# Kernel tuning notes

Hardware: AMD Instinct MI355X
Metric: run time of the kernel (lower is better)

## Reference

```python
import jax, jax.numpy as jnp
from jax import lax
import numpy as np

DN = ('NCHW', 'OIHW', 'NCHW')

def _conv(x, w, b, s):
    # torch Conv2d(kernel=3, padding=1, stride=s)
    y = lax.conv_general_dilated(x, w, (s, s), ((1, 1), (1, 1)), dimension_numbers=DN)
    return y + b[None, :, None, None]

def _convT(x, w, b, s):
    # torch ConvTranspose2d weight layout [in, out, kh, kw]; kernel=3, padding=1, output_padding=s-1
    wk = jnp.flip(w, (2, 3)).transpose(1, 0, 2, 3)  # -> OIHW
    y = lax.conv_general_dilated(x, wk, (1, 1), ((1, s), (1, s)), lhs_dilation=(s, s), dimension_numbers=DN)
    return y + b[None, :, None, None]

def _inorm(x, eps=1e-5):
    # torch InstanceNorm2d (affine=False)
    m = jnp.mean(x, (2, 3), keepdims=True)
    v = jnp.var(x, (2, 3), keepdims=True)
    return (x - m) * lax.rsqrt(v + eps)

def _prelu(x, a):
    return jnp.where(x >= 0, x, a * x)

def _block(x, w, b, a, s):
    return _prelu(_inorm(_conv(x, w, b, s)), a)

def _sage(x, src, tgt, wl, bl, wr, n):
    # PyG SAGEConv, mean aggregation: lin_l(scatter_mean(x[src] -> tgt)) + lin_r(x)
    deg = jnp.zeros((n,), x.dtype).at[tgt].add(1.0)
    agg = jnp.zeros((x.shape[0], n, x.shape[2]), x.dtype).at[:, tgt].add(x[:, src])
    agg = agg / jnp.maximum(deg, 1.0)[None, :, None]
    return jnp.einsum('bnc,oc->bno', agg, wl) + bl + jnp.einsum('bnc,oc->bno', x, wr)

def setup_inputs() -> dict:
    keys = iter(jax.random.split(jax.random.key(0), 64))
    def rn(shape, s=0.05):
        return jax.random.normal(next(keys), shape, jnp.float32) * s
    inp = {}
    inp['x'] = jax.random.normal(next(keys), (16, 1, 400, 400), jnp.float32)
    inp['edges'] = jax.random.randint(next(keys), (2, 5000), 0, 625, jnp.int32)
    for name, (ci, co) in zip(['d4', 'd3', 'd2', 'd1'], [(1, 32), (32, 64), (64, 128), (128, 256)]):
        inp['w_' + name] = rn((co, ci, 3, 3)); inp['b_' + name] = rn((co,))
        inp['a_' + name] = jnp.full((1,), 0.25, jnp.float32)
    inp['w_bot'] = rn((256, 256, 3, 3)); inp['b_bot'] = rn((256,))
    inp['a_bot'] = jnp.full((1,), 0.25, jnp.float32)
    for i in ['1', '2']:
        inp['wl' + i] = rn((256, 256)); inp['bl' + i] = rn((256,)); inp['wr' + i] = rn((256, 256))
    for name, (ci, co) in zip(['u1', 'u2', 'u3'], [(512, 128), (256, 64), (128, 32)]):
        inp['w_' + name] = rn((ci, co, 3, 3)); inp['b_' + name] = rn((co,))
        inp['a_' + name] = jnp.full((1,), 0.25, jnp.float32)
    inp['w_u4'] = rn((64, 2, 3, 3)); inp['b_u4'] = rn((2,))
    return inp

def reference(x, edges, w_d4, b_d4, a_d4, w_d3, b_d3, a_d3, w_d2, b_d2, a_d2, w_d1, b_d1, a_d1, w_bot, b_bot, a_bot, wl1, bl1, wr1, wl2, bl2, wr2, w_u1, b_u1, a_u1, w_u2, b_u2, a_u2, w_u3, b_u3, a_u3, w_u4, b_u4):
    xs = []
    x = _block(x, w_d4, b_d4, a_d4, 2); xs.append(x)   # [B,32,200,200]
    x = _block(x, w_d3, b_d3, a_d3, 2); xs.append(x)   # [B,64,100,100]
    x = _block(x, w_d2, b_d2, a_d2, 2); xs.append(x)   # [B,128,50,50]
    x = _block(x, w_d1, b_d1, a_d1, 2); xs.append(x)   # [B,256,25,25]
    x = _block(x, w_bot, b_bot, a_bot, 1)              # [B,256,25,25]
    B = x.shape[0]
    x = x.reshape(B, 256, -1).transpose(0, 2, 1)       # [B,625,256]
    src, tgt = edges[0], edges[1]
    x = jax.nn.relu(_sage(x, src, tgt, wl1, bl1, wr1, 625))
    x = jax.nn.relu(_sage(x, src, tgt, wl2, bl2, wr2, 625))
    x = x.transpose(0, 2, 1).reshape(B, 256, 25, 25)
    x = jnp.concatenate([xs[3], x], 1)                 # 512 ch
    x = _prelu(_inorm(_convT(x, w_u1, b_u1, 2)), a_u1) # [B,128,50,50]
    x = jnp.concatenate([xs[2], x], 1)
    x = _prelu(_inorm(_convT(x, w_u2, b_u2, 2)), a_u2) # [B,64,100,100]
    x = jnp.concatenate([xs[1], x], 1)
    x = _prelu(_inorm(_convT(x, w_u3, b_u3, 2)), a_u3) # [B,32,200,200]
    x = jnp.concatenate([xs[0], x], 1)
    return _convT(x, w_u4, b_u4, 2)                    # [B,2,400,400], conv_only top
```

## Files before the change

kernel.cpp:

```cpp
#include <hip/hip_runtime.h>
#include <hip/hip_bf16.h>

typedef __hip_bfloat16 bf16;

typedef __bf16 bf16x8 __attribute__((ext_vector_type(8)));
typedef float  f32x16 __attribute__((ext_vector_type(16)));

static __device__ __forceinline__ float bf(const bf16 v){ return __bfloat162float(v); }
static __device__ __forceinline__ float bfu(unsigned short u){
  unsigned fw = ((unsigned)u) << 16; float v; __builtin_memcpy(&v, &fw, 4); return v;
}

static __device__ __forceinline__ float ldm(const void* p, long i, int f){
  return f ? ((const float*)p)[i] : __bfloat162float(((const bf16*)p)[i]);
}
static __device__ __forceinline__ void stm(void* p, long i, int f, float v){
  if(f) ((float*)p)[i] = v; else ((bf16*)p)[i] = __float2bfloat16(v);
}
static __device__ __forceinline__ unsigned short bfbits(float v){
  __hip_bfloat16 h = __float2bfloat16(v);
  return *(unsigned short*)&h;
}

__global__ void k_detect(const void* __restrict__ w, int* __restrict__ mode){
  if(blockIdx.x == 0 && threadIdx.x == 0){
    const unsigned int* u = (const unsigned int*)w;
    int saneLo = 0;
    for(int i = 0; i < 64; i++){
      unsigned short lo = (unsigned short)(u[i] & 0xFFFFu);
      unsigned int fw = ((unsigned int)lo) << 16;
      float v; __builtin_memcpy(&v, &fw, 4);
      float a = fabsf(v);
      if(a > 1e-7f && a < 100.f) saneLo++;
    }
    *mode = (saneLo >= 48) ? 0 : 1;
  }
}

__global__ void k_wtrans6(const void* __restrict__ w, bf16* __restrict__ wF,
                          const int* __restrict__ dmode){
  int idx = blockIdx.x * 256 + threadIdx.x;
  if(idx >= 65536) return;
  int dm = *dmode;
  int e = idx & 7;
  int L = (idx >> 3) & 63;
  int r = idx >> 9;
  int nc = r & 7;
  int kc = r >> 3;
  int o = nc*32 + (L & 31);
  int c = kc*16 + (L >> 5)*8 + e;
  wF[idx] = __float2bfloat16(ldm(w, (long)o*256 + c, dm));
}

__global__ void k_wtrans4(const void* __restrict__ w, bf16* __restrict__ wF,
                          const int* __restrict__ dmode, int Cin, int Cout){
  int idx = blockIdx.x * 256 + threadIdx.x;
  if(idx >= Cin * Cout * 9) return;
  int dm = *dmode;
  int e = idx & 7;
  int L = (idx >> 3) & 63;
  int r = idx >> 9;
  int NC = Cout >> 5;
  int nc = r % NC; r /= NC;
  int t  = r % 9;
  int kc = r / 9;
  int ci = kc*16 + (L>>5)*8 + e;
  int co = nc*32 + (L&31);
  wF[idx] = __float2bfloat16(ldm(w, ((long)ci*Cout + co)*9 + t, dm));
}

__global__ void k_wtrans5(const void* __restrict__ w, bf16* __restrict__ wF,
                          const int* __restrict__ dmode, int Cin, int Cout){
  int idx = blockIdx.x * 256 + threadIdx.x;
  if(idx >= Cin * Cout * 9) return;
  int dm = *dmode;
  int e = idx & 7;
  int L = (idx >> 3) & 63;
  int r = idx >> 9;
  int NC = Cout >> 5;
  int nc = r % NC; r /= NC;
  int t  = r % 9;
  int kc = r / 9;
  int ci = kc*16 + (L>>5)*8 + e;
  int co = nc*32 + (L&31);
  wF[idx] = __float2bfloat16(ldm(w, ((long)co*Cin + ci)*9 + t, dm));
}

__global__ void k_count(const int* __restrict__ tgt, int* __restrict__ icur, int E){
  int e = blockIdx.x * 256 + threadIdx.x;
  if(e < E) atomicAdd(&icur[tgt[e]], 1);
}
__global__ void k_scan(int* __restrict__ icur, int* __restrict__ off, int N){
  if(blockIdx.x == 0 && threadIdx.x == 0){
    int acc = 0;
    for(int i = 0; i < N; i++){ off[i] = acc; acc += icur[i]; icur[i] = 0; }
    off[N] = acc;
  }
}
__global__ void k_place(const int* __restrict__ src, const int* __restrict__ tgt,
                        const int* __restrict__ off, int* __restrict__ icur,
                        int* __restrict__ eidx, int E){
  int e = blockIdx.x * 256 + threadIdx.x;
  if(e < E){
    int d = tgt[e];
    int p = atomicAdd(&icur[d], 1);
    eidx[off[d] + p] = src[e];
  }
}

__global__ __launch_bounds__(256, 4)
void k_conv_d4(const void* __restrict__ in, long in_off,
               const void* __restrict__ w, const void* __restrict__ bias,
               bf16* __restrict__ out, const int* __restrict__ dmode)
{
  __shared__ float sW[288];
  __shared__ float sB[32];
  int tid = threadIdx.x;
  int dm = *dmode;
  for(int e = tid; e < 288; e += 256) sW[e] = ldm(w, e, dm);
  if(tid < 32)  sB[tid] = ldm(bias, tid, dm);
  __syncthreads();
  int r = tid / 50, jt = tid % 50;
  if(r >= 5) return;
  int ho = blockIdx.x * 5 + r;
  int b  = blockIdx.z;
  int j0 = jt * 4;

  float x[3][9];
  long ibase = in_off + (long)b * 160000;
  #pragma unroll
  for(int rr = 0; rr < 3; rr++){
    int ir = 2*ho - 1 + rr;
    if(ir < 0 || ir >= 400){
      #pragma unroll
      for(int c = 0; c < 9; c++) x[rr][c] = 0.f;
      continue;
    }
    long rb = ibase + (long)ir * 400;
    int c0 = 2*j0 - 1;
    #pragma unroll
    for(int c = 0; c < 9; c++){
      int ic = c0 + c;
      x[rr][c] = (ic >= 0 && ic < 400) ? ldm(in, rb + ic, dm) : 0.f;
    }
  }

  long obase = ((long)b * 32) * 40000 + (long)ho * 200 + j0;
  for(int co = 0; co < 32; co++){
    const float* wv = &sW[co*9];
    float bv = sB[co];
    float a[4];
    #pragma unroll
    for(int p = 0; p < 4; p++){
      float s = bv;
      #pragma unroll
      for(int kh = 0; kh < 3; kh++)
        #pragma unroll
        for(int kw = 0; kw < 3; kw++)
          s += x[kh][2*p + kw] * wv[kh*3 + kw];
      a[p] = s;
    }
    ushort4 pk;
    pk.x = bfbits(a[0]); pk.y = bfbits(a[1]); pk.z = bfbits(a[2]); pk.w = bfbits(a[3]);
    *(ushort4*)&out[obase + (long)co * 40000] = pk;
  }
}

template<int CW, int NWC, int NWM, int S, int OCC, int VECW>
__global__ __launch_bounds__(256, OCC)
void k_convSM(const void* __restrict__ in, long in_off, int fin_sel,
              const bf16* __restrict__ wF, const void* __restrict__ bias,
              void* __restrict__ out, int fout,
              const int* __restrict__ dmode,
              int Cin, int Hin, int Win, int Cout, int Hout, int Wout, int nym)
{
  constexpr int CP = 40;
  constexpr int HALF = CW/2;
  __shared__ unsigned short sX[3*CW*CP];
  int tid  = threadIdx.x;
  int lane = tid & 63;
  int wv   = tid >> 6;
  int nc   = wv % NWC;
  int mt   = wv / NWC;
  int ho   = blockIdx.x;
  int colg = blockIdx.y % nym;
  int cog  = blockIdx.y / nym;
  int b    = blockIdx.z;
  int dm   = *dmode;
  int fin  = (fin_sel == 2) ? dm : fin_sel;
  int NCtot = Cout >> 5;
  int chunk = cog*NWC + nc;
  int jl   = mt*32 + (lane & 31);
  int hi   = lane >> 5;
  int C0   = S*(colg*NWM*32);
  int ir0  = S*ho - 1;

  f32x16 acc;
  #pragma unroll
  for(int q = 0; q < 16; q++) acc[q] = 0.f;

  int p0, p1, p2;
  if(S == 2){ p0 = jl; p1 = HALF + jl; p2 = jl + 1; }
  else      { p0 = jl; p1 = jl + 1;    p2 = jl + 2; }

  for(int ci0 = 0; ci0 < Cin; ci0 += 32){
    if(VECW == 1){
      for(int e = tid; e < 12*CW; e += 256){
        int c  = e % CW;
        int s  = e / CW;
        int kg = s & 3, r = s >> 2;
        int ir = ir0 + r;
        int ic = C0 - 1 + c;
        unsigned pk0, pk1, pk2, pk3;
        if(ir >= 0 && ir < Hin && ic >= 0 && ic < Win){
          long step = (long)Hin*Win;
          long base = in_off + ((long)b*Cin + ci0 + kg*8)*step + (long)ir*Win + ic;
          unsigned short t8[8];
          #pragma unroll
          for(int u = 0; u < 8; u++) t8[u] = bfbits(ldm(in, base + u*step, fin));
          pk0 = t8[0] | ((unsigned)t8[1]<<16);
          pk1 = t8[2] | ((unsigned)t8[3]<<16);
          pk2 = t8[4] | ((unsigned)t8[5]<<16);
          pk3 = t8[6] | ((unsigned)t8[7]<<16);
        } else { pk0=0; pk1=0; pk2=0; pk3=0; }
        int pos = (S == 2) ? ((c&1) ? HALF + (c>>1) : (c>>1)) : c;
        uint4 q; q.x=pk0; q.y=pk1; q.z=pk2; q.w=pk3;
        *(uint4*)&sX[(r*CW + pos)*CP + kg*8] = q;
      }
    } else {
      const unsigned short* bp = (const unsigned short*)in;
      long step = (long)Hin*Win;
      int L0 = (C0 >= 1) ? ((C0-1) & ~(VECW-1)) : -VECW;
      int ng = (C0 + CW - 2 - L0)/VECW + 1;
      int total = 3 * 8 * ng;
      for(int e = tid; e < total; e += 256){
        int c4 = e & 7;
        int s  = e >> 3;
        int g  = s % ng;
        int r  = s / ng;
        int ir = ir0 + r;
        int L  = L0 + g*VECW;
        int cib = ci0 + c4*4;
        unsigned short t[4][VECW];
        if(ir >= 0 && ir < Hin && L >= 0 && L + VECW <= Win){
          const unsigned short* rp = bp + in_off + ((long)b*Cin + cib)*step + (long)ir*Win + L;
          #pragma unroll
          for(int u = 0; u < 4; u++){
            if(VECW == 4){
              ushort4 v = *(const ushort4*)(rp + u*step);
              t[u][0]=v.x; t[u][1]=v.y; t[u][2]=v.z; t[u][3]=v.w;
            } else {
              ushort2 v = *(const ushort2*)(rp + u*step);
              t[u][0]=v.x; t[u][1]=v.y;
            }
          }
        } else {
          #pragma unroll
          for(int j = 0; j < VECW; j++){
            int ic = L + j;
            bool ok = (ir >= 0 && ir < Hin && ic >= 0 && ic < Win);
            #pragma unroll
            for(int u = 0; u < 4; u++)
              t[u][j] = ok ? bp[in_off + ((long)b*Cin + cib+u)*step + (long)ir*Win + ic]
                           : (unsigned short)0;
          }
        }
        #pragma unroll
        for(int j = 0; j < VECW; j++){
          int c = L - C0 + 1 + j;
          if(c < 0 || c >= CW) continue;
          int pos = (S == 2) ? ((c&1) ? HALF + (c>>1) : (c>>1)) : c;
          uint2 q;
          q.x = t[0][j] | ((unsigned)t[1][j]<<16);
          q.y = t[2][j] | ((unsigned)t[3][j]<<16);
          *(uint2*)&sX[(r*CW + pos)*CP + c4*4] = q;
        }
      }
    }
    __syncthreads();

    #pragma unroll
    for(int kg2 = 0; kg2 < 2; kg2++){
      int kbase = 8*hi + kg2*16;
      bf16x8 x[9];
      #pragma unroll
      for(int r = 0; r < 3; r++){
        x[r*3+0] = *(const bf16x8*)&sX[(r*CW + p0)*CP + kbase];
        x[r*3+1] = *(const bf16x8*)&sX[(r*CW + p1)*CP + kbase];
        x[r*3+2] = *(const bf16x8*)&sX[(r*CW + p2)*CP + kbase];
      }
      int kc = (ci0 >> 4) + kg2;
      const bf16x8* wb = ((const bf16x8*)wF) + ((long)(kc*9)*NCtot + chunk)*64 + lane;
      const long ws = (long)NCtot*64;
      #pragma unroll
      for(int t = 0; t < 9; t++){
        bf16x8 w = wb[(long)t*ws];
        acc = __builtin_amdgcn_mfma_f32_32x32x16_bf16(w, x[t], acc, 0,0,0);
      }
    }
    __syncthreads();
  }

  int j = colg*NWM*32 + jl;
  if(j < Wout){
    #pragma unroll
    for(int r16 = 0; r16 < 16; r16++){
      int co = chunk*32 + (r16&3) + 8*(r16>>2) + 4*hi;
      float bv = ldm(bias, co, dm);
      stm(out, ((long)b*Cout + co)*Hout*Wout + (long)ho*Wout + j, fout, acc[r16] + bv);
    }
  }
}

__global__ void k_inorm_prelu(void* __restrict__ x, int f, int HW,
                              const void* __restrict__ a, const int* __restrict__ dmode)
{
  int dm = *dmode;
  long base = (long)blockIdx.x * HW;
  float s = 0.f, s2 = 0.f;
  int vec = (f == 0) && ((HW & 3) == 0);
  if(vec){
    const ushort4* vp = (const ushort4*)((const bf16*)x + base);
    int n = HW >> 2;
    for(int i = threadIdx.x; i < n; i += 256){
      ushort4 v = vp[i];
      float a0 = bfu(v.x), a1 = bfu(v.y), a2 = bfu(v.z), a3 = bfu(v.w);
      s  += (a0 + a1) + (a2 + a3);
      s2 += (a0*a0 + a1*a1) + (a2*a2 + a3*a3);
    }
  } else {
    for(int i = threadIdx.x; i < HW; i += 256){ float v = ldm(x, base + i, f); s += v; s2 += v*v; }
  }
  __shared__ float sh[256], sh2[256];
  sh[threadIdx.x] = s; sh2[threadIdx.x] = s2; __syncthreads();
  for(int off = 128; off > 0; off >>= 1){
    if(threadIdx.x < off){ sh[threadIdx.x] += sh[threadIdx.x+off]; sh2[threadIdx.x] += sh2[threadIdx.x+off]; }
    __syncthreads();
  }
  float mean = sh[0] / HW;
  float var  = sh2[0] / HW - mean * mean;
  float inv  = rsqrtf(fmaxf(var, 0.f) + 1e-5f);
  float alpha = ldm(a, 0, dm);
  if(vec){
    ushort4* vp = (ushort4*)((bf16*)x + base);
    int n = HW >> 2;
    for(int i = threadIdx.x; i < n; i += 256){
      ushort4 v = vp[i];
      float t[4] = { bfu(v.x), bfu(v.y), bfu(v.z), bfu(v.w) };
      #pragma unroll
      for(int k = 0; k < 4; k++){
        float u = (t[k] - mean) * inv;
        t[k] = u >= 0.f ? u : alpha * u;
      }
      ushort4 o;
      o.x = bfbits(t[0]); o.y = bfbits(t[1]); o.z = bfbits(t[2]); o.w = bfbits(t[3]);
      vp[i] = o;
    }
  } else {
    for(int i = threadIdx.x; i < HW; i += 256){
      float v = (ldm(x, base + i, f) - mean) * inv;
      stm(x, base + i, f, v >= 0.f ? v : alpha * v);
    }
  }
}

__global__ void k_transpose(const float* __restrict__ in, float* __restrict__ out, int B, int C, int N){
  long idx = (long)blockIdx.x * 256 + threadIdx.x;
  long total = (long)B * C * N; if(idx >= total) return;
  int c = (int)(idx % C); long t = idx / C; int n = (int)(t % N); int b = (int)(t / N);
  out[idx] = in[((long)b * C + c) * N + n];
}

__global__ __launch_bounds__(256, 4)
void k_sageG(const float* __restrict__ xT,
             const int* __restrict__ off, const int* __restrict__ eidx,
             const bf16* __restrict__ wlF, const bf16* __restrict__ wrF,
             const void* __restrict__ bl,
             float* __restrict__ out, const int* __restrict__ dmode,
             int NROW, int trans)
{
  constexpr int CP = 264;
  __shared__ unsigned short sS[2*32*CP];
  int tid  = threadIdx.x;
  int lane = tid & 63;
  int wv   = tid >> 6;
  int ln   = lane & 31;
  int hi   = lane >> 5;
  int n0   = blockIdx.x * 32;
  int og0  = blockIdx.y * 128;
  int ncg  = blockIdx.y*4 + wv;
  int dm   = *dmode;

  for(int e = tid; e < 4096; e += 256){
    int c4 = e & 63;
    int r  = (e >> 6) & 31;
    int ar = e >> 11;
    int row = n0 + r;
    unsigned pk0 = 0, pk1 = 0;
    if(row < NROW){
      float4 v;
      if(ar == 0){
        v = *(const float4*)&xT[(long)row*256 + c4*4];
      } else {
        int b = row / 625;
        int n = row - b*625;
        int s0 = off[n], s1 = off[n+1];
        v.x = 0.f; v.y = 0.f; v.z = 0.f; v.w = 0.f;
        long bb = (long)b*625*256 + c4*4;
        for(int k = s0; k < s1; k++){
          int s = eidx[k];
          float4 u = *(const float4*)&xT[bb + (long)s*256];
          v.x += u.x; v.y += u.y; v.z += u.z; v.w += u.w;
        }
        float dinv = 1.0f / fmaxf((float)(s1 - s0), 1.0f);
        v.x *= dinv; v.y *= dinv; v.z *= dinv; v.w *= dinv;
      }
      pk0 = bfbits(v.x) | ((unsigned)bfbits(v.y) << 16);
      pk1 = bfbits(v.z) | ((unsigned)bfbits(v.w) << 16);
    }
    uint2 q; q.x = pk0; q.y = pk1;
    *(uint2*)&sS[(ar*32 + r)*CP + c4*4] = q;
  }
  __syncthreads();

  f32x16 acc;
  #pragma unroll
  for(int q = 0; q < 16; q++) acc[q] = 0.f;

  int xb = ln*CP + 8*hi;
  #pragma unroll
  for(int kc = 0; kc < 16; kc++){
    bf16x8 bx = *(const bf16x8*)&sS[xb + kc*16];
    bf16x8 ba = *(const bf16x8*)&sS[32*CP + xb + kc*16];
    bf16x8 wl = ((const bf16x8*)wlF)[(long)(kc*8 + ncg)*64 + lane];
    bf16x8 wr = ((const bf16x8*)wrF)[(long)(kc*8 + ncg)*64 + lane];
    acc = __builtin_amdgcn_mfma_f32_32x32x16_bf16(wl, ba, acc, 0,0,0);
    acc = __builtin_amdgcn_mfma_f32_32x32x16_bf16(wr, bx, acc, 0,0,0);
  }

  if(trans){
    int row = n0 + ln;
    if(row < NROW){
      int b = row / 625, n = row - b*625;
      #pragma unroll
      for(int r16 = 0; r16 < 16; r16++){
        int o = ncg*32 + (r16&3) + 8*(r16>>2) + 4*hi;
        float v = acc[r16] + ldm(bl, o, dm);
        out[((long)b*256 + o)*625 + n] = fmaxf(v, 0.f);
      }
    }
  } else {
    float* sO = (float*)sS;
    __syncthreads();
    #pragma unroll
    for(int r16 = 0; r16 < 16; r16++){
      int ol = wv*32 + (r16&3) + 8*(r16>>2) + 4*hi;
      float v = acc[r16] + ldm(bl, og0 + ol, dm);
      sO[ln*130 + ol] = fmaxf(v, 0.f);
    }
    __syncthreads();
    for(int e = tid; e < 4096; e += 256){
      int r = e >> 7, oc = e & 127;
      int row = n0 + r;
      if(row < NROW) out[(long)row*256 + og0 + oc] = sO[r*130 + oc];
    }
  }
}

template<int CW, int NWC, int NWM, int CC, int CIP, int VECW>
__global__ __launch_bounds__(512, 4)
void k_convTG(const void* __restrict__ inA, int fA,
              const void* __restrict__ inB, int fB,
              const bf16* __restrict__ wF, const void* __restrict__ bias,
              bf16* __restrict__ out, const int* __restrict__ dmode,
              int Hin, int Win, int Cout)
{
  __shared__ unsigned short sX[4*CW*CIP];
  int tid  = threadIdx.x;
  int lane = tid & 63;
  int wv   = tid >> 6;
  int low  = wv & 3;
  int h    = wv >> 2;
  int nc   = low % NWC;
  int mt   = low / NWC;
  int j0   = mt * 32;
  int i    = blockIdx.x;
  int b    = blockIdx.z;
  int dm   = *dmode;
  int ln   = lane & 31;
  int hi   = lane >> 5;
  int NCtot = Cout >> 5;

  f32x16 acc0, acc1, acc2, acc3;
  #pragma unroll
  for(int q = 0; q < 16; q++){ acc0[q]=0.f; acc1[q]=0.f; acc2[q]=0.f; acc3[q]=0.f; }

  if(VECW == 1){
    for(int e = tid; e < 4*CW*(CC/8); e += 512){
      int col = e % CW;
      int s   = e / CW;
      int kg  = s % (CC/8); s /= (CC/8);
      int row = s & 1;
      int hf  = s >> 1;
      int ii  = i + row;
      unsigned pk0=0, pk1=0, pk2=0, pk3=0;
      if(ii < Hin && col < Win){
        const void* sp = hf ? inB : inA;
        int ff = hf ? fB : fA;
        long step = (long)Hin*Win;
        long base = ((long)b*CC + kg*8)*step + (long)ii*Win + col;
        unsigned short t8[8];
        #pragma unroll
        for(int u = 0; u < 8; u++) t8[u] = bfbits(ldm(sp, base + u*step, ff));
        pk0 = t8[0] | ((unsigned)t8[1]<<16);
        pk1 = t8[2] | ((unsigned)t8[3]<<16);
        pk2 = t8[4] | ((unsigned)t8[5]<<16);
        pk3 = t8[6] | ((unsigned)t8[7]<<16);
      }
      uint4 q; q.x=pk0; q.y=pk1; q.z=pk2; q.w=pk3;
      *(uint4*)&sX[((hf*2 + row)*CW + col)*CIP + kg*8] = q;
    }
  } else {
    long step = (long)Hin*Win;
    constexpr int NG = (CW + VECW - 1)/VECW;
    constexpr int NC4 = CC/4;
    int total = 4 * NC4 * NG;
    for(int e = tid; e < total; e += 512){
      int c4 = e % NC4;
      int s  = e / NC4;
      int g  = s % NG; s /= NG;
      int row = s & 1;
      int hf  = s >> 1;
      int ii  = i + row;
      int col0 = g*VECW;
      const unsigned short* bp = (const unsigned short*)(hf ? inB : inA);
      unsigned short t[4][VECW];
      if(ii < Hin && col0 + VECW <= Win){
        const unsigned short* rp = bp + ((long)b*CC + c4*4)*step + (long)ii*Win + col0;
        #pragma unroll
        for(int u = 0; u < 4; u++){
          if(VECW == 4){
            ushort4 v = *(const ushort4*)(rp + u*step);
            t[u][0]=v.x; t[u][1]=v.y; t[u][2]=v.z; t[u][3]=v.w;
          } else {
            ushort2 v = *(const ushort2*)(rp + u*step);
            t[u][0]=v.x; t[u][1]=v.y;
          }
        }
      } else {
        #pragma unroll
        for(int j = 0; j < VECW; j++){
          int ic = col0 + j;
          bool ok = (ii < Hin && ic < Win);
          #pragma unroll
          for(int u = 0; u < 4; u++)
            t[u][j] = ok ? bp[((long)b*CC + c4*4+u)*step + (long)ii*Win + ic]
                         : (unsigned short)0;
        }
      }
      #pragma unroll
      for(int j = 0; j < VECW; j++){
        int c = col0 + j;
        if(c >= CW) continue;
        uint2 q;
        q.x = t[0][j] | ((unsigned)t[1][j]<<16);
        q.y = t[2][j] | ((unsigned)t[3][j]<<16);
        *(uint2*)&sX[((hf*2 + row)*CW + c)*CIP + c4*4] = q;
      }
    }
  }
  __syncthreads();

  for(int kc = 0; kc < CC/16; kc++){
    int kb = kc*16 + 8*hi;
    bf16x8 x00 = *(const bf16x8*)&sX[((h*2+0)*CW + j0 + ln)*CIP + kb];
    bf16x8 x01 = *(const bf16x8*)&sX[((h*2+0)*CW + j0 + ln + 1)*CIP + kb];
    bf16x8 x10 = *(const bf16x8*)&sX[((h*2+1)*CW + j0 + ln)*CIP + kb];
    bf16x8 x11 = *(const bf16x8*)&sX[((h*2+1)*CW + j0 + ln + 1)*CIP + kb];
    int kcg = h*(CC/16) + kc;
    const bf16x8* wb = ((const bf16x8*)wF) + ((long)(kcg*9)*NCtot + nc)*64 + lane;
    const int ws = NCtot*64;
    bf16x8 w0=wb[0],    w1=wb[ws],   w2=wb[2*ws], w3=wb[3*ws], w4=wb[4*ws],
           w5=wb[5*ws], w6=wb[6*ws], w7=wb[7*ws], w8=wb[8*ws];
    acc0 = __builtin_amdgcn_mfma_f32_32x32x16_bf16(w4, x00, acc0, 0,0,0);
    acc1 = __builtin_amdgcn_mfma_f32_32x32x16_bf16(w5, x00, acc1, 0,0,0);
    acc1 = __builtin_amdgcn_mfma_f32_32x32x16_bf16(w3, x01, acc1, 0,0,0);
    acc2 = __builtin_amdgcn_mfma_f32_32x32x16_bf16(w7, x00, acc2, 0,0,0);
    acc2 = __builtin_amdgcn_mfma_f32_32x32x16_bf16(w1, x10, acc2, 0,0,0);
    acc3 = __builtin_amdgcn_mfma_f32_32x32x16_bf16(w8, x00, acc3, 0,0,0);
    acc3 = __builtin_amdgcn_mfma_f32_32x32x16_bf16(w6, x01, acc3, 0,0,0);
    acc3 = __builtin_amdgcn_mfma_f32_32x32x16_bf16(w2, x10, acc3, 0,0,0);
    acc3 = __builtin_amdgcn_mfma_f32_32x32x16_bf16(w0, x11, acc3, 0,0,0);
  }

  float* sR = (float*)sX;
  __syncthreads();
  if(h == 1){
    #pragma unroll
    for(int q = 0; q < 16; q++){
      sR[(0*16+q)*256 + low*64 + lane] = acc0[q];
      sR[(1*16+q)*256 + low*64 + lane] = acc1[q];
      sR[(2*16+q)*256 + low*64 + lane] = acc2[q];
      sR[(3*16+q)*256 + low*64 + lane] = acc3[q];
    }
  }
  __syncthreads();
  if(h == 0){
    #pragma unroll
    for(int q = 0; q < 16; q++){
      acc0[q] += sR[(0*16+q)*256 + low*64 + lane];
      acc1[q] += sR[(1*16+q)*256 + low*64 + lane];
      acc2[q] += sR[(2*16+q)*256 + low*64 + lane];
      acc3[q] += sR[(3*16+q)*256 + low*64 + lane];
    }
    int j = j0 + ln;
    if(j < Win){
      int Wout = 2*Win;
      #pragma unroll
      for(int r = 0; r < 16; r++){
        int co = nc*32 + (r&3) + 8*(r>>2) + 4*hi;
        float bv = ldm(bias, co, dm);
        long base0 = (((long)b*Cout + co)*2*Hin + 2*i)*(long)Wout + 2*j;
        unsigned p0 = bfbits(acc0[r]+bv) | ((unsigned)bfbits(acc1[r]+bv) << 16);
        unsigned p1 = bfbits(acc2[r]+bv) | ((unsigned)bfbits(acc3[r]+bv) << 16);
        *(unsigned*)&out[base0]        = p0;
        *(unsigned*)&out[base0 + Wout] = p1;
      }
    }
  }
}

__global__ __launch_bounds__(256, 4)
void k_convT8(const bf16* __restrict__ inA, const bf16* __restrict__ inB,
              const void* __restrict__ w, const void* __restrict__ bias,
              void* __restrict__ out, long out_off, int fout_sel,
              const int* __restrict__ dmode, int Hin, int Win)
{
  __shared__ float sW[64*2*9];
  __shared__ float sB[2];
  int tid = threadIdx.x;
  int dm = *dmode;
  for(int e = tid; e < 64*2*9; e += 256) sW[e] = ldm(w, e, dm);
  if(tid < 2) sB[tid] = ldm(bias, tid, dm);
  __syncthreads();
  int r  = tid / 50;
  int jt = tid % 50;
  if(r >= 5) return;
  int i  = blockIdx.x * 5 + r;
  int b  = blockIdx.z;
  int j0 = jt * 4;
  int fout = (fout_sel == 2) ? dm : fout_sel;

  float acc[2][4][4];
  #pragma unroll
  for(int co = 0; co < 2; co++)
    #pragma unroll
    for(int p = 0; p < 4; p++){
      acc[co][p][0]=0.f; acc[co][p][1]=0.f; acc[co][p][2]=0.f; acc[co][p][3]=0.f;
    }

  bool e4   = (j0 + 4 < Win);
  bool row1 = (i + 1 < Hin);

  for(int ci = 0; ci < 64; ci++){
    const bf16* src = (ci < 32) ? inA : inB;
    int cc = ci & 31;
    const bf16* rp = src + ((long)b*32 + cc)*(long)Hin*Win + (long)i*Win + j0;
    float x0[5], x1[5];
    ushort4 v0 = *(const ushort4*)rp;
    x0[0]=bfu(v0.x); x0[1]=bfu(v0.y); x0[2]=bfu(v0.z); x0[3]=bfu(v0.w);
    x0[4] = e4 ? bf(rp[4]) : 0.f;
    if(row1){
      ushort4 v1 = *(const ushort4*)(rp + Win);
      x1[0]=bfu(v1.x); x1[1]=bfu(v1.y); x1[2]=bfu(v1.z); x1[3]=bfu(v1.w);
      x1[4] = e4 ? bf(rp[Win + 4]) : 0.f;
    } else {
      x1[0]=0.f; x1[1]=0.f; x1[2]=0.f; x1[3]=0.f; x1[4]=0.f;
    }
    const float* wp = &sW[ci*18];
    float wv[18];
    #pragma unroll
    for(int k = 0; k < 18; k++) wv[k] = wp[k];
    #pragma unroll
    for(int p = 0; p < 4; p++){
      float a00 = x0[p], a01 = x0[p+1], a10 = x1[p], a11 = x1[p+1];
      #pragma unroll
      for(int co = 0; co < 2; co++){
        const float* wc = &wv[co*9];
        acc[co][p][0] += a00*wc[4];
        acc[co][p][1] += a00*wc[5] + a01*wc[3];
        acc[co][p][2] += a00*wc[7] + a10*wc[1];
        acc[co][p][3] += a00*wc[8] + a01*wc[6] + a10*wc[2] + a11*wc[0];
      }
    }
  }
  int Wout = 2*Win;
  #pragma unroll
  for(int co = 0; co < 2; co++){
    float bv = sB[co];
    long base = out_off + (((long)b*2 + co)*2*Hin + 2*i)*(long)Wout + 2*j0;
    #pragma unroll
    for(int p = 0; p < 4; p++){
      stm(out, base + 2*p,            fout, acc[co][p][0] + bv);
      stm(out, base + 2*p + 1,        fout, acc[co][p][1] + bv);
      stm(out, base + 2*p + Wout,     fout, acc[co][p][2] + bv);
      stm(out, base + 2*p + Wout + 1, fout, acc[co][p][3] + bv);
    }
  }
}

static inline int cdiv(long a, long b){ return (int)((a + b - 1) / b); }

extern "C" void kernel_launch(void* const* d_in, const int* in_sizes, int n_in,
                              void* d_out, int out_size, void* d_ws, size_t ws_size,
                              hipStream_t stream) {
  const void* x_in  = d_in[0];
  const int*  edges = (const int*)d_in[1];
  const int* src = edges;
  const int* tgt = edges + 5000;
  const void *w_d4=d_in[2],  *b_d4=d_in[3],  *a_d4=d_in[4];
  const void *w_d3=d_in[5],  *b_d3=d_in[6],  *a_d3=d_in[7];
  const void *w_d2=d_in[8],  *b_d2=d_in[9],  *a_d2=d_in[10];
  const void *w_d1=d_in[11], *b_d1=d_in[12], *a_d1=d_in[13];
  const void *w_bot=d_in[14],*b_bot=d_in[15],*a_bot=d_in[16];
  const void *wl1=d_in[17], *bl1=d_in[18], *wr1=d_in[19];
  const void *wl2=d_in[20], *bl2=d_in[21], *wr2=d_in[22];
  const void *w_u1=d_in[23], *b_u1=d_in[24], *a_u1=d_in[25];
  const void *w_u2=d_in[26], *b_u2=d_in[27], *a_u2=d_in[28];
  const void *w_u3=d_in[29], *b_u3=d_in[30], *a_u3=d_in[31];
  const void *w_u4=d_in[32], *b_u4=d_in[33];

  const int NNODE = 625, E = 5000, CG = 256;

  const long TAIL = 4096 + 4*262144L + (589824L + 147456L + 36864L) * 2 + 32768;
  const long ENCW = 976896L * 2;
  int Bc = 16;
  while(Bc > 1 && (7680000L * Bc + TAIL) > (long)ws_size) Bc >>= 1;
  int enc_in_pool = (Bc >= 8);
  if(!enc_in_pool){
    Bc = 16;
    while(Bc > 1 && (7680000L * Bc + TAIL + ENCW) > (long)ws_size) Bc >>= 1;
  }

  char* wsb = (char*)d_ws;
  long o_xs1  = 2560000L * Bc;
  long o_BIGA = 3840000L * Bc;
  long o_BIGB = 6400000L * Bc;
  long o_deg  = 7680000L * Bc;
  bf16*  xs0 = (bf16*)wsb;
  bf16*  xs1 = (bf16*)(wsb + o_xs1);
  bf16*  xs2 = (bf16*)(wsb + o_BIGA);
  bf16*  xs3 = (bf16*)(wsb + o_BIGA +  640000L*Bc);
  float* bot = (float*)(wsb + o_BIGA +  960000L*Bc);
  float* xT  = (float*)(wsb + o_BIGA + 1600000L*Bc);
  bf16*  u1  = (bf16*)(wsb + o_BIGA + 1600000L*Bc);
  bf16*  u3  = (bf16*)(wsb + o_BIGA);
  float* g1  = (float*)(wsb + o_BIGB +  640000L*Bc);
  bf16*  u2  = (bf16*)(wsb + o_BIGB);
  int*  mode = (int*)(wsb + o_deg + 3072);
  bf16*  wlF1 = (bf16*)(wsb + o_deg + 4096);
  bf16*  wrF1 = wlF1 + 65536;
  bf16*  wlF2 = wrF1 + 65536;
  bf16*  wrF2 = wlF2 + 65536;
  bf16*  wTu1 = (bf16*)(wsb + o_deg + 4096 + 4*262144L);
  bf16*  wTu2 = wTu1 + 589824;
  bf16*  wTu3 = wTu2 + 147456;
  int*   ioff = (int*)(wTu3 + 36864);
  int*   icur = ioff + 626;
  int*   eidx = icur + 625;
  bf16*  wTd3 = enc_in_pool ? (bf16*)(wsb + o_BIGA + 2240000L*Bc) : (bf16*)(eidx + 5000);
  bf16*  wTd2 = wTd3 + 18432;
  bf16*  wTd1 = wTd2 + 73728;
  bf16*  wTdB = wTd1 + 294912;
  float* g2  = bot;

  hipLaunchKernelGGL(k_detect, dim3(1), dim3(1), 0, stream, w_d4, mode);

  hipMemsetAsync(icur, 0, NNODE*sizeof(int), stream);
  hipLaunchKernelGGL(k_count, dim3(cdiv(E,256)), dim3(256), 0, stream, tgt, icur, E);
  hipLaunchKernelGGL(k_scan,  dim3(1), dim3(64), 0, stream, icur, ioff, NNODE);
  hipLaunchKernelGGL(k_place, dim3(cdiv(E,256)), dim3(256), 0, stream, src, tgt, ioff, icur, eidx, E);

  hipLaunchKernelGGL(k_wtrans6, dim3(256), dim3(256), 0, stream, wl1, wlF1, mode);
  hipLaunchKernelGGL(k_wtrans6, dim3(256), dim3(256), 0, stream, wr1, wrF1, mode);
  hipLaunchKernelGGL(k_wtrans6, dim3(256), dim3(256), 0, stream, wl2, wlF2, mode);
  hipLaunchKernelGGL(k_wtrans6, dim3(256), dim3(256), 0, stream, wr2, wrF2, mode);
  hipLaunchKernelGGL(k_wtrans4, dim3(cdiv(589824,256)), dim3(256), 0, stream, w_u1, wTu1, mode, 512, 128);
  hipLaunchKernelGGL(k_wtrans4, dim3(cdiv(147456,256)), dim3(256), 0, stream, w_u2, wTu2, mode, 256, 64);
  hipLaunchKernelGGL(k_wtrans4, dim3(cdiv(36864,256)),  dim3(256), 0, stream, w_u3, wTu3, mode, 128, 32);

  for(int bo = 0; bo < 16; bo += Bc){
    long x_off   = (long)bo * 160000;
    long out_off = (long)bo * 320000;

    hipLaunchKernelGGL(k_wtrans5, dim3(cdiv(18432,256)),  dim3(256), 0, stream, w_d3, wTd3, mode, 32, 64);
    hipLaunchKernelGGL(k_wtrans5, dim3(cdiv(73728,256)),  dim3(256), 0, stream, w_d2, wTd2, mode, 64, 128);
    hipLaunchKernelGGL(k_wtrans5, dim3(cdiv(294912,256)), dim3(256), 0, stream, w_d1, wTd1, mode, 128, 256);
    hipLaunchKernelGGL(k_wtrans5, dim3(cdiv(589824,256)), dim3(256), 0, stream, w_bot, wTdB, mode, 256, 256);

    hipLaunchKernelGGL(k_conv_d4, dim3(40, 1, Bc), dim3(256), 0, stream,
                       x_in, x_off, w_d4, b_d4, xs0, mode);
    hipLaunchKernelGGL(k_inorm_prelu, dim3(Bc*32), dim3(256), 0, stream, xs0, 0, 40000, a_d4, mode);
    hipLaunchKernelGGL((k_convSM<130,2,2,2,4,4>), dim3(100, 2, Bc), dim3(256), 0, stream,
                       xs0, 0L, 0, wTd3, b_d3, xs1, 0, mode, 32, 200, 200, 64, 100, 100, 2);
    hipLaunchKernelGGL(k_inorm_prelu, dim3(Bc*64), dim3(256), 0, stream, xs1, 0, 10000, a_d3, mode);
    hipLaunchKernelGGL((k_convSM<66,4,1,2,4,4>), dim3(50, 2, Bc), dim3(256), 0, stream,
                       xs1, 0L, 0, wTd2, b_d2, xs2, 0, mode, 64, 100, 100, 128, 50, 50, 2);
    hipLaunchKernelGGL(k_inorm_prelu, dim3(Bc*128), dim3(256), 0, stream, xs2, 0, 2500, a_d2, mode);
    hipLaunchKernelGGL((k_convSM<66,4,1,2,4,2>), dim3(25, 2, Bc), dim3(256), 0, stream,
                       xs2, 0L, 0, wTd1, b_d1, xs3, 0, mode, 128, 50, 50, 256, 25, 25, 1);
    hipLaunchKernelGGL(k_inorm_prelu, dim3(Bc*256), dim3(256), 0, stream, xs3, 0, 625, a_d1, mode);
    hipLaunchKernelGGL((k_convSM<34,4,1,1,4,1>), dim3(25, 2, Bc), dim3(256), 0, stream,
                       xs3, 0L, 0, wTdB, b_bot, bot, 1, mode, 256, 25, 25, 256, 25, 25, 1);
    hipLaunchKernelGGL(k_inorm_prelu, dim3(Bc*256), dim3(256), 0, stream, bot, 1, 625, a_bot, mode);

    { long n = (long)Bc*CG*NNODE;
      hipLaunchKernelGGL(k_transpose, dim3(cdiv(n,256)), dim3(256), 0, stream, bot, xT, Bc, CG, NNODE); }
    hipLaunchKernelGGL(k_sageG, dim3(cdiv((long)Bc*NNODE,32), 2), dim3(256), 0, stream,
                       xT, ioff, eidx, wlF1, wrF1, bl1, g1, mode, Bc*NNODE, 0);
    hipLaunchKernelGGL(k_sageG, dim3(cdiv((long)Bc*NNODE,32), 2), dim3(256), 0, stream,
                       g1, ioff, eidx, wlF2, wrF2, bl2, g2, mode, Bc*NNODE, 1);

    hipLaunchKernelGGL((k_convTG<34,4,1,256,264,1>), dim3(25, 1, Bc), dim3(512), 0, stream,
                       xs3, 0, g2, 1, wTu1, b_u1, u1, mode, 25, 25, 128);
    hipLaunchKernelGGL(k_inorm_prelu, dim3(Bc*128), dim3(256), 0, stream, u1, 0, 2500, a_u1, mode);
    hipLaunchKernelGGL((k_convTG<66,2,2,128,136,2>), dim3(50, 1, Bc), dim3(512), 0, stream,
                       xs2, 0, u1, 0, wTu2, b_u2, u2, mode, 50, 50, 64);
    hipLaunchKernelGGL(k_inorm_prelu, dim3(Bc*64), dim3(256), 0, stream, u2, 0, 10000, a_u2, mode);
    hipLaunchKernelGGL((k_convTG<130,1,4,64,72,4>), dim3(100, 1, Bc), dim3(512), 0, stream,
                       xs1, 0, u2, 0, wTu3, b_u3, u3, mode, 100, 100, 32);
    hipLaunchKernelGGL(k_inorm_prelu, dim3(Bc*32), dim3(256), 0, stream, u3, 0, 40000, a_u3, mode);
    hipLaunchKernelGGL(k_convT8, dim3(40, 1, Bc), dim3(256), 0, stream,
                       xs0, u3, w_u4, b_u4, d_out, out_off, 2, mode, 200, 200);
  }
}
```

Measured before the change: 904.0 us.

## Fuse instance-norm statistics into conv epilogues via atomic per-channel sums

Conv and transposed-conv epilogues now reduce per-channel sum and sum-of-squares across each wave with shuffles and accumulate them into a global stats buffer using atomics. The instance-norm kernel reads these precomputed stats instead of re-reading the whole activation tensor for its reduction pass, which removes one full read per normalized layer. In exchange it adds shuffle reductions and many float atomics in the conv epilogues, a memset per batch chunk, and statistics rounded in fp32 before the bf16 store, with nondeterministic summation order.

After: 1.568 ms. +73.5%, slower.

```diff
diff --git a/kernel.cpp b/kernel.cpp
--- a/kernel.cpp
+++ b/kernel.cpp
@@ -172,7 +172,8 @@
               const bf16* __restrict__ wF, const void* __restrict__ bias,
               void* __restrict__ out, int fout,
               const int* __restrict__ dmode,
-              int Cin, int Hin, int Win, int Cout, int Hout, int Wout, int nym)
+              int Cin, int Hin, int Win, int Cout, int Hout, int Wout, int nym,
+              float* __restrict__ stats)
 {
   constexpr int CP = 40;
   constexpr int HALF = CW/2;
@@ -192,6 +193,7 @@
   int chunk = cog*NWC + nc;
   int jl   = mt*32 + (lane & 31);
   int hi   = lane >> 5;
+  int ln   = lane & 31;
   int C0   = S*(colg*NWM*32);
   int ir0  = S*ho - 1;
 
@@ -302,43 +304,61 @@
   }
 
   int j = colg*NWM*32 + jl;
-  if(j < Wout){
-    #pragma unroll
-    for(int r16 = 0; r16 < 16; r16++){
-      int co = chunk*32 + (r16&3) + 8*(r16>>2) + 4*hi;
-      float bv = ldm(bias, co, dm);
-      stm(out, ((long)b*Cout + co)*Hout*Wout + (long)ho*Wout + j, fout, acc[r16] + bv);
+  bool act = (j < Wout);
+  #pragma unroll
+  for(int r16 = 0; r16 < 16; r16++){
+    int co = chunk*32 + (r16&3) + 8*(r16>>2) + 4*hi;
+    float bv = ldm(bias, co, dm);
+    float v = acc[r16] + bv;
+    if(act) stm(out, ((long)b*Cout + co)*Hout*Wout + (long)ho*Wout + j, fout, v);
+    if(stats){
+      float c  = act ? v : 0.f;
+      float c2 = c*c;
+      #pragma unroll
+      for(int o = 1; o < 32; o <<= 1){ c += __shfl_xor(c, o); c2 += __shfl_xor(c2, o); }
+      if(ln == 0){
+        atomicAdd(&stats[((long)b*Cout + co)*2],     c);
+        atomicAdd(&stats[((long)b*Cout + co)*2 + 1], c2);
+      }
     }
   }
 }
 
 __global__ void k_inorm_prelu(void* __restrict__ x, int f, int HW,
-                              const void* __restrict__ a, const int* __restrict__ dmode)
+                              const void* __restrict__ a, const int* __restrict__ dmode,
+                              const float* __restrict__ stats)
 {
   int dm = *dmode;
   long base = (long)blockIdx.x * HW;
-  float s = 0.f, s2 = 0.f;
   int vec = (f == 0) && ((HW & 3) == 0);
-  if(vec){
-    const ushort4* vp = (const ushort4*)((const bf16*)x + base);
-    int n = HW >> 2;
-    for(int i = threadIdx.x; i < n; i += 256){
-      ushort4 v = vp[i];
-      float a0 = bfu(v.x), a1 = bfu(v.y), a2 = bfu(v.z), a3 = bfu(v.w);
-      s  += (a0 + a1) + (a2 + a3);
-      s2 += (a0*a0 + a1*a1) + (a2*a2 + a3*a3);
-    }
+  float mean, var;
+  if(stats){
+    float s = stats[(long)blockIdx.x*2], s2 = stats[(long)blockIdx.x*2 + 1];
+    mean = s / HW;
+    var  = s2 / HW - mean * mean;
   } else {
-    for(int i = threadIdx.x; i < HW; i += 256){ float v = ldm(x, base + i, f); s += v; s2 += v*v; }
-  }
-  __shared__ float sh[256], sh2[256];
-  sh[threadIdx.x] = s; sh2[threadIdx.x] = s2; __syncthreads();
-  for(int off = 128; off > 0; off >>= 1){
-    if(threadIdx.x < off){ sh[threadIdx.x] += sh[threadIdx.x+off]; sh2[threadIdx.x] += sh2[threadIdx.x+off]; }
-    __syncthreads();
-  }
-  float mean = sh[0] / HW;
-  float var  = sh2[0] / HW - mean * mean;
+    float s = 0.f, s2 = 0.f;
+    if(vec){
+      const ushort4* vp = (const ushort4*)((const bf16*)x + base);
+      int n = HW >> 2;
+      for(int i = threadIdx.x; i < n; i += 256){
+        ushort4 v = vp[i];
+        float a0 = bfu(v.x), a1 = bfu(v.y), a2 = bfu(v.z), a3 = bfu(v.w);
+        s  += (a0 + a1) + (a2 + a3);
+        s2 += (a0*a0 + a1*a1) + (a2*a2 + a3*a3);
+      }
+    } else {
+      for(int i = threadIdx.x; i < HW; i += 256){ float v = ldm(x, base + i, f); s += v; s2 += v*v; }
+    }
+    __shared__ float sh[256], sh2[256];
+    sh[threadIdx.x] = s; sh2[threadIdx.x] = s2; __syncthreads();
+    for(int off = 128; off > 0; off >>= 1){
+      if(threadIdx.x < off){ sh[threadIdx.x] += sh[threadIdx.x+off]; sh2[threadIdx.x] += sh2[threadIdx.x+off]; }
+      __syncthreads();
+    }
+    mean = sh[0] / HW;
+    var  = sh2[0] / HW - mean * mean;
+  }
   float inv  = rsqrtf(fmaxf(var, 0.f) + 1e-5f);
   float alpha = ldm(a, 0, dm);
   if(vec){
@@ -473,7 +493,7 @@
               const void* __restrict__ inB, int fB,
               const bf16* __restrict__ wF, const void* __restrict__ bias,
               bf16* __restrict__ out, const int* __restrict__ dmode,
-              int Hin, int Win, int Cout)
+              int Hin, int Win, int Cout, float* __restrict__ stats)
 {
   __shared__ unsigned short sX[4*CW*CIP];
   int tid  = threadIdx.x;
@@ -614,17 +634,29 @@
       acc3[q] += sR[(3*16+q)*256 + low*64 + lane];
     }
     int j = j0 + ln;
-    if(j < Win){
-      int Wout = 2*Win;
-      #pragma unroll
-      for(int r = 0; r < 16; r++){
-        int co = nc*32 + (r&3) + 8*(r>>2) + 4*hi;
-        float bv = ldm(bias, co, dm);
+    bool act = (j < Win);
+    int Wout = 2*Win;
+    #pragma unroll
+    for(int r = 0; r < 16; r++){
+      int co = nc*32 + (r&3) + 8*(r>>2) + 4*hi;
+      float bv = ldm(bias, co, dm);
+      float v0 = acc0[r]+bv, v1 = acc1[r]+bv, v2 = acc2[r]+bv, v3 = acc3[r]+bv;
+      if(act){
         long base0 = (((long)b*Cout + co)*2*Hin + 2*i)*(long)Wout + 2*j;
-        unsigned p0 = bfbits(acc0[r]+bv) | ((unsigned)bfbits(acc1[r]+bv) << 16);
-        unsigned p1 = bfbits(acc2[r]+bv) | ((unsigned)bfbits(acc3[r]+bv) << 16);
+        unsigned p0 = bfbits(v0) | ((unsigned)bfbits(v1) << 16);
+        unsigned p1 = bfbits(v2) | ((unsigned)bfbits(v3) << 16);
         *(unsigned*)&out[base0]        = p0;
         *(unsigned*)&out[base0 + Wout] = p1;
+      }
+      if(stats){
+        float c  = act ? (v0 + v1 + v2 + v3) : 0.f;
+        float c2 = act ? (v0*v0 + v1*v1 + v2*v2 + v3*v3) : 0.f;
+        #pragma unroll
+        for(int o = 1; o < 32; o <<= 1){ c += __shfl_xor(c, o); c2 += __shfl_xor(c2, o); }
+        if(ln == 0){
+          atomicAdd(&stats[((long)b*Cout + co)*2],     c);
+          atomicAdd(&stats[((long)b*Cout + co)*2 + 1], c2);
+        }
       }
     }
   }
@@ -732,7 +764,7 @@
 
   const int NNODE = 625, E = 5000, CG = 256;
 
-  const long TAIL = 4096 + 4*262144L + (589824L + 147456L + 36864L) * 2 + 32768;
+  const long TAIL = 4096 + 4*262144L + (589824L + 147456L + 36864L) * 2 + 32768 + 131072;
   const long ENCW = 976896L * 2;
   int Bc = 16;
   while(Bc > 1 && (7680000L * Bc + TAIL) > (long)ws_size) Bc >>= 1;
@@ -768,7 +800,15 @@
   int*   ioff = (int*)(wTu3 + 36864);
   int*   icur = ioff + 626;
   int*   eidx = icur + 625;
-  bf16*  wTd3 = enc_in_pool ? (bf16*)(wsb + o_BIGA + 2240000L*Bc) : (bf16*)(eidx + 5000);
+  float* st_xs1 = (float*)(eidx + 5000);
+  float* st_xs2 = st_xs1 + 16*64*2;
+  float* st_xs3 = st_xs2 + 16*128*2;
+  float* st_bot = st_xs3 + 16*256*2;
+  float* st_u1  = st_bot + 16*256*2;
+  float* st_u2  = st_u1  + 16*128*2;
+  float* st_u3  = st_u2  + 16*64*2;
+  long   st_total = 16L*2*(64+128+256+256+128+64+32);
+  bf16*  wTd3 = enc_in_pool ? (bf16*)(wsb + o_BIGA + 2240000L*Bc) : (bf16*)(st_xs1 + st_total);
   bf16*  wTd2 = wTd3 + 18432;
   bf16*  wTd1 = wTd2 + 73728;
   bf16*  wTdB = wTd1 + 294912;
@@ -793,6 +833,8 @@
     long x_off   = (long)bo * 160000;
     long out_off = (long)bo * 320000;
 
+    hipMemsetAsync(st_xs1, 0, st_total*sizeof(float), stream);
+
     hipLaunchKernelGGL(k_wtrans5, dim3(cdiv(18432,256)),  dim3(256), 0, stream, w_d3, wTd3, mode, 32, 64);
     hipLaunchKernelGGL(k_wtrans5, dim3(cdiv(73728,256)),  dim3(256), 0, stream, w_d2, wTd2, mode, 64, 128);
     hipLaunchKernelGGL(k_wtrans5, dim3(cdiv(294912,256)), dim3(256), 0, stream, w_d1, wTd1, mode, 128, 256);
@@ -800,19 +842,19 @@
 
     hipLaunchKernelGGL(k_conv_d4, dim3(40, 1, Bc), dim3(256), 0, stream,
                        x_in, x_off, w_d4, b_d4, xs0, mode);
-    hipLaunchKernelGGL(k_inorm_prelu, dim3(Bc*32), dim3(256), 0, stream, xs0, 0, 40000, a_d4, mode);
+    hipLaunchKernelGGL(k_inorm_prelu, dim3(Bc*32), dim3(256), 0, stream, xs0, 0, 40000, a_d4, mode, (const float*)nullptr);
     hipLaunchKernelGGL((k_convSM<130,2,2,2,4,4>), dim3(100, 2, Bc), dim3(256), 0, stream,
-                       xs0, 0L, 0, wTd3, b_d3, xs1, 0, mode, 32, 200, 200, 64, 100, 100, 2);
-    hipLaunchKernelGGL(k_inorm_prelu, dim3(Bc*64), dim3(256), 0, stream, xs1, 0, 10000, a_d3, mode);
+                       xs0, 0L, 0, wTd3, b_d3, xs1, 0, mode, 32, 200, 200, 64, 100, 100, 2, st_xs1);
+    hipLaunchKernelGGL(k_inorm_prelu, dim3(Bc*64), dim3(256), 0, stream, xs1, 0, 10000, a_d3, mode, st_xs1);
     hipLaunchKernelGGL((k_convSM<66,4,1,2,4,4>), dim3(50, 2, Bc), dim3(256), 0, stream,
-                       xs1, 0L, 0, wTd2, b_d2, xs2, 0, mode, 64, 100, 100, 128, 50, 50, 2);
-    hipLaunchKernelGGL(k_inorm_prelu, dim3(Bc*128), dim3(256), 0, stream, xs2, 0, 2500, a_d2, mode);
+                       xs1, 0L, 0, wTd2, b_d2, xs2, 0, mode, 64, 100, 100, 128, 50, 50, 2, st_xs2);
+    hipLaunchKernelGGL(k_inorm_prelu, dim3(Bc*128), dim3(256), 0, stream, xs2, 0, 2500, a_d2, mode, st_xs2);
     hipLaunchKernelGGL((k_convSM<66,4,1,2,4,2>), dim3(25, 2, Bc), dim3(256), 0, stream,
-                       xs2, 0L, 0, wTd1, b_d1, xs3, 0, mode, 128, 50, 50, 256, 25, 25, 1);
-    hipLaunchKernelGGL(k_inorm_prelu, dim3(Bc*256), dim3(256), 0, stream, xs3, 0, 625, a_d1, mode);
+                       xs2, 0L, 0, wTd1, b_d1, xs3, 0, mode, 128, 50, 50, 256, 25, 25, 1, st_xs3);
+    hipLaunchKernelGGL(k_inorm_prelu, dim3(Bc*256), dim3(256), 0, stream, xs3, 0, 625, a_d1, mode, st_xs3);
     hipLaunchKernelGGL((k_convSM<34,4,1,1,4,1>), dim3(25, 2, Bc), dim3(256), 0, stream,
-                       xs3, 0L, 0, wTdB, b_bot, bot, 1, mode, 256, 25, 25, 256, 25, 25, 1);
-    hipLaunchKernelGGL(k_inorm_prelu, dim3(Bc*256), dim3(256), 0, stream, bot, 1, 625, a_bot, mode);
+                       xs3, 0L, 0, wTdB, b_bot, bot, 1, mode, 256, 25, 25, 256, 25, 25, 1, st_bot);
+    hipLaunchKernelGGL(k_inorm_prelu, dim3(Bc*256), dim3(256), 0, stream, bot, 1, 625, a_bot, mode, st_bot);
 
     { long n = (long)Bc*CG*NNODE;
       hipLaunchKernelGGL(k_transpose, dim3(cdiv(n,256)), dim3(256), 0, stream, bot, xT, Bc, CG, NNODE); }
@@ -822,14 +864,14 @@
                        g1, ioff, eidx, wlF2, wrF2, bl2, g2, mode, Bc*NNODE, 1);
 
     hipLaunchKernelGGL((k_convTG<34,4,1,256,264,1>), dim3(25, 1, Bc), dim3(512), 0, stream,
-                       xs3, 0, g2, 1, wTu1, b_u1, u1, mode, 25, 25, 128);
-    hipLaunchKernelGGL(k_inorm_prelu, dim3(Bc*128), dim3(256), 0, stream, u1, 0, 2500, a_u1, mode);
+                       xs3, 0, g2, 1, wTu1, b_u1, u1, mode, 25, 25, 128, st_u1);
+    hipLaunchKernelGGL(k_inorm_prelu, dim3(Bc*128), dim3(256), 0, stream, u1, 0, 2500, a_u1, mode, st_u1);
     hipLaunchKernelGGL((k_convTG<66,2,2,128,136,2>), dim3(50, 1, Bc), dim3(512), 0, stream,
-                       xs2, 0, u1, 0, wTu2, b_u2, u2, mode, 50, 50, 64);
-    hipLaunchKernelGGL(k_inorm_prelu, dim3(Bc*64), dim3(256), 0, stream, u2, 0, 10000, a_u2, mode);
+                       xs2, 0, u1, 0, wTu2, b_u2, u2, mode, 50, 50, 64, st_u2);
+    hipLaunchKernelGGL(k_inorm_prelu, dim3(Bc*64), dim3(256), 0, stream, u2, 0, 10000, a_u2, mode, st_u2);
     hipLaunchKernelGGL((k_convTG<130,1,4,64,72,4>), dim3(100, 1, Bc), dim3(512), 0, stream,
-                       xs1, 0, u2, 0, wTu3, b_u3, u3, mode, 100, 100, 32);
-    hipLaunchKernelGGL(k_inorm_prelu, dim3(Bc*32), dim3(256), 0, stream, u3, 0, 40000, a_u3, mode);
+                       xs1, 0, u2, 0, wTu3, b_u3, u3, mode, 100, 100, 32, st_u3);
+    hipLaunchKernelGGL(k_inorm_prelu, dim3(Bc*32), dim3(256), 0, stream, u3, 0, 40000, a_u3, mode, st_u3);
     hipLaunchKernelGGL(k_convT8, dim3(40, 1, Bc), dim3(256), 0, stream,
                        xs0, u3, w_u4, b_u4, d_out, out_off, 2, mode, 200, 200);
   }
```
